# Optimization experiments

Measured on AMD Instinct MI355X. Metric: run time of the kernel, lower is better.

Reference implementation:

```python
import jax, jax.numpy as jnp
import numpy as np

B, N = 2048, 100            # batch, n_atoms
NC2 = N * (N - 1) // 2      # 4950 strictly-lower-triangle pairs

# Row-major strictly-lower-triangle indices: (1,0),(2,0),(2,1),(3,0),...
# This matches tf.where over band_part(index_matrix,-1,0)-diag in Triangle.
_TRIL_R, _TRIL_C = np.tril_indices(N, k=-1)


def setup_inputs() -> dict:
    key = jax.random.key(0)
    k1, k2 = jax.random.split(key)
    coords = jax.random.normal(k1, (B, N, 3), dtype=jnp.float32)
    decompFE_flat = jax.random.normal(k2, (B, NC2), dtype=jnp.float32)
    return {"coords": coords, "decompFE_flat": decompFE_flat}


def _triangle(flat):
    """[B, NC2] -> symmetric [B, N, N] with zero diagonal (Q + Q^T)."""
    b = flat.shape[0]
    m = jnp.zeros((b, N, N), dtype=flat.dtype).at[:, _TRIL_R, _TRIL_C].set(flat)
    return m + jnp.swapaxes(m, 1, 2)


def reference(coords, decompFE_flat):
    # Symmetric decomposed pairwise energies [B, N, N]
    decompFE = _triangle(decompFE_flat)

    # Pairwise squared distances [B, N, N]
    diff = coords[:, :, None, :] - coords[:, None, :, :]
    diff2 = jnp.sum(diff * diff, axis=-1)

    # Strictly-lower-triangle distances in row-major order [B, NC2]
    # (TF extracts nonzeros of the lower band; off-diagonal distances are
    #  nonzero for generic coords, so this is exactly the strict lower tri.)
    r_flat = jnp.sqrt(diff2[:, _TRIL_R, _TRIL_C])
    recip_r_flat = 1.0 / r_flat

    # Symmetric 1/r matrix, then einsum 'bijk,bij->bk' with k=1 == full ij sum
    Q3 = _triangle(recip_r_flat)
    E = jnp.sum(Q3 * decompFE, axis=(1, 2), keepdims=True)[:, :, 0] / 2.0  # [B,1]
    return E
```

## Files before the change

### kernel.cpp

```cpp
#include <hip/hip_runtime.h>


#define BATCH 2048
#define NATOMS 100
#define NPAIRS 4950
#define BLOCK 256

__global__ __launch_bounds__(BLOCK) void eij_kernel(
    const float* __restrict__ coords,
    const float* __restrict__ decomp,
    float* __restrict__ out)
{
    __shared__ float sx[NATOMS];
    __shared__ float sy[NATOMS];
    __shared__ float sz[NATOMS];
    __shared__ float wave_sums[BLOCK / 64];

    const int b = blockIdx.x;
    const int t = threadIdx.x;

    const float* cb = coords + (size_t)b * NATOMS * 3;
    for (int i = t; i < NATOMS; i += BLOCK) {
        sx[i] = cb[i * 3 + 0];
        sy[i] = cb[i * 3 + 1];
        sz[i] = cb[i * 3 + 2];
    }
    __syncthreads();

    const float* db = decomp + (size_t)b * NPAIRS;
    float acc = 0.0f;

    for (int p = t; p < NPAIRS; p += BLOCK) {
        int i = (int)((1.0f + sqrtf(8.0f * (float)p + 1.0f)) * 0.5f);
        while (i * (i - 1) / 2 > p) --i;
        while ((i + 1) * i / 2 <= p) ++i;
        const int j = p - i * (i - 1) / 2;

        const float dx = sx[i] - sx[j];
        const float dy = sy[i] - sy[j];
        const float dz = sz[i] - sz[j];
        const float d2 = dx * dx + dy * dy + dz * dz;
        acc += db[p] * rsqrtf(d2);
    }

    #pragma unroll
    for (int off = 32; off > 0; off >>= 1)
        acc += __shfl_down(acc, off, 64);

    const int wave = t >> 6;
    const int lane = t & 63;
    if (lane == 0) wave_sums[wave] = acc;
    __syncthreads();

    if (t == 0) {
        float s = 0.0f;
        #pragma unroll
        for (int w = 0; w < BLOCK / 64; ++w) s += wave_sums[w];
        out[b] = s;
    }
}

extern "C" void kernel_launch(void* const* d_in, const int* in_sizes, int n_in,
                              void* d_out, int out_size, void* d_ws, size_t ws_size,
                              hipStream_t stream) {
    const float* coords = (const float*)d_in[0];
    const float* decomp = (const float*)d_in[1];
    float* out = (float*)d_out;

    eij_kernel<<<BATCH, BLOCK, 0, stream>>>(coords, decomp, out);
}
```

Baseline: 91.34 us.

## Replace per-pair index solve with constexpr pair table and unroll loads

Precomputes a compile-time table mapping each flat pair index to packed (i,j) bytes, which replaces the sqrt plus correction-loop inversion done per element. Atom coordinates are stored as float4 in shared memory so each atom needs one LDS read. The pair loop is fully unrolled to a fixed 20 iterations with predicated tail handling so loads can be issued early. The cost is extra global/constant reads of the 16-bit table and higher register pressure from unrolling.

```diff
diff --git a/kernel.cpp b/kernel.cpp
--- a/kernel.cpp
+++ b/kernel.cpp
@@ -5,59 +5,69 @@
 #define NATOMS 100
 #define NPAIRS 4950
 #define BLOCK 256
+#define KMAX 20
+
+struct PairTab { unsigned short v[NPAIRS]; };
+
+__host__ __device__ constexpr PairTab make_tab() {
+    PairTab t{};
+    int p = 0;
+    for (int i = 1; i < NATOMS; ++i)
+        for (int j = 0; j < i; ++j)
+            t.v[p++] = (unsigned short)((i << 8) | j);
+    return t;
+}
+
+__device__ constexpr PairTab PAIR_TAB = make_tab();
 
 __global__ __launch_bounds__(BLOCK) void eij_kernel(
     const float* __restrict__ coords,
     const float* __restrict__ decomp,
     float* __restrict__ out)
 {
-    __shared__ float sx[NATOMS];
-    __shared__ float sy[NATOMS];
-    __shared__ float sz[NATOMS];
+    __shared__ float4 satom[NATOMS];
     __shared__ float wave_sums[BLOCK / 64];
 
     const int b = blockIdx.x;
     const int t = threadIdx.x;
 
     const float* cb = coords + (size_t)b * NATOMS * 3;
-    for (int i = t; i < NATOMS; i += BLOCK) {
-        sx[i] = cb[i * 3 + 0];
-        sy[i] = cb[i * 3 + 1];
-        sz[i] = cb[i * 3 + 2];
+    if (t < NATOMS) {
+        satom[t] = make_float4(cb[t * 3 + 0], cb[t * 3 + 1], cb[t * 3 + 2], 0.0f);
     }
     __syncthreads();
 
     const float* db = decomp + (size_t)b * NPAIRS;
     float acc = 0.0f;
 
-    for (int p = t; p < NPAIRS; p += BLOCK) {
-        int i = (int)((1.0f + sqrtf(8.0f * (float)p + 1.0f)) * 0.5f);
-        while (i * (i - 1) / 2 > p) --i;
-        while ((i + 1) * i / 2 <= p) ++i;
-        const int j = p - i * (i - 1) / 2;
-
-        const float dx = sx[i] - sx[j];
-        const float dy = sy[i] - sy[j];
-        const float dz = sz[i] - sz[j];
+    #pragma unroll
+    for (int k = 0; k < KMAX; ++k) {
+        const int p = t + (k << 8);
+        const bool ok = (p < NPAIRS);
+        const int pp = ok ? p : 0;
+        const float d = db[pp];
+        const unsigned pr = PAIR_TAB.v[pp];
+        const int i = (int)(pr >> 8);
+        const int j = (int)(pr & 255u);
+        const float4 ci = satom[i];
+        const float4 cj = satom[j];
+        const float dx = ci.x - cj.x;
+        const float dy = ci.y - cj.y;
+        const float dz = ci.z - cj.z;
         const float d2 = dx * dx + dy * dy + dz * dz;
-        acc += db[p] * rsqrtf(d2);
+        const float contrib = d * rsqrtf(d2);
+        acc += ok ? contrib : 0.0f;
     }
 
     #pragma unroll
     for (int off = 32; off > 0; off >>= 1)
         acc += __shfl_down(acc, off, 64);
 
-    const int wave = t >> 6;
-    const int lane = t & 63;
-    if (lane == 0) wave_sums[wave] = acc;
+    if ((t & 63) == 0) wave_sums[t >> 6] = acc;
     __syncthreads();
 
-    if (t == 0) {
-        float s = 0.0f;
-        #pragma unroll
-        for (int w = 0; w < BLOCK / 64; ++w) s += wave_sums[w];
-        out[b] = s;
-    }
+    if (t == 0)
+        out[b] = wave_sums[0] + wave_sums[1] + wave_sums[2] + wave_sums[3];
 }
 
 extern "C" void kernel_launch(void* const* d_in, const int* in_sizes, int n_in,
```

Measured after the change: 81.98 us. -10.2%, faster.

## Map waves to triangle rows and lanes to columns, dropping index inversion

Applied to the files above, without the earlier changes.

The per-pair sqrt-based triangular index inversion is replaced by a row-per-wave loop: each wave takes rows i strided by the wave count, and each lane handles columns lane and lane+64. Each lane keeps its two j-atom coordinates in registers, and row coordinates come from a shared-memory broadcast. This removes the sqrt, the correction loops and the scattered LDS gathers for j. In exchange, short rows leave lanes idle, and the work across waves is somewhat unbalanced.

```diff
diff --git a/kernel.cpp b/kernel.cpp
--- a/kernel.cpp
+++ b/kernel.cpp
@@ -5,59 +5,62 @@
 #define NATOMS 100
 #define NPAIRS 4950
 #define BLOCK 256
+#define NWAVES (BLOCK / 64)
 
 __global__ __launch_bounds__(BLOCK) void eij_kernel(
     const float* __restrict__ coords,
     const float* __restrict__ decomp,
     float* __restrict__ out)
 {
-    __shared__ float sx[NATOMS];
-    __shared__ float sy[NATOMS];
-    __shared__ float sz[NATOMS];
-    __shared__ float wave_sums[BLOCK / 64];
+    __shared__ float sx[NATOMS], sy[NATOMS], sz[NATOMS];
+    __shared__ float wave_sums[NWAVES];
 
     const int b = blockIdx.x;
     const int t = threadIdx.x;
+    const int wave = t >> 6;
+    const int lane = t & 63;
 
     const float* cb = coords + (size_t)b * NATOMS * 3;
-    for (int i = t; i < NATOMS; i += BLOCK) {
-        sx[i] = cb[i * 3 + 0];
-        sy[i] = cb[i * 3 + 1];
-        sz[i] = cb[i * 3 + 2];
+    for (int a = t; a < NATOMS; a += BLOCK) {
+        sx[a] = cb[a * 3 + 0];
+        sy[a] = cb[a * 3 + 1];
+        sz[a] = cb[a * 3 + 2];
     }
     __syncthreads();
+
+    const int j1 = (lane + 64 < NATOMS) ? (lane + 64) : (NATOMS - 1);
+    const float x0 = sx[lane], y0 = sy[lane], z0 = sz[lane];
+    const float x1 = sx[j1],   y1 = sy[j1],   z1 = sz[j1];
 
     const float* db = decomp + (size_t)b * NPAIRS;
     float acc = 0.0f;
 
-    for (int p = t; p < NPAIRS; p += BLOCK) {
-        int i = (int)((1.0f + sqrtf(8.0f * (float)p + 1.0f)) * 0.5f);
-        while (i * (i - 1) / 2 > p) --i;
-        while ((i + 1) * i / 2 <= p) ++i;
-        const int j = p - i * (i - 1) / 2;
+    for (int i = wave + 1; i < NATOMS; i += NWAVES) {
+        const int base = i * (i - 1) / 2;
+        const float cix = sx[i];
+        const float ciy = sy[i];
+        const float ciz = sz[i];
 
-        const float dx = sx[i] - sx[j];
-        const float dy = sy[i] - sy[j];
-        const float dz = sz[i] - sz[j];
-        const float d2 = dx * dx + dy * dy + dz * dz;
-        acc += db[p] * rsqrtf(d2);
+        if (lane < i) {
+            const float d = db[base + lane];
+            const float dx = cix - x0, dy = ciy - y0, dz = ciz - z0;
+            acc += d * rsqrtf(dx * dx + dy * dy + dz * dz);
+        }
+        if (lane + 64 < i) {
+            const float d = db[base + 64 + lane];
+            const float dx = cix - x1, dy = ciy - y1, dz = ciz - z1;
+            acc += d * rsqrtf(dx * dx + dy * dy + dz * dz);
+        }
     }
 
     #pragma unroll
     for (int off = 32; off > 0; off >>= 1)
         acc += __shfl_down(acc, off, 64);
-
-    const int wave = t >> 6;
-    const int lane = t & 63;
     if (lane == 0) wave_sums[wave] = acc;
     __syncthreads();
 
-    if (t == 0) {
-        float s = 0.0f;
-        #pragma unroll
-        for (int w = 0; w < BLOCK / 64; ++w) s += wave_sums[w];
-        out[b] = s;
-    }
+    if (t == 0)
+        out[b] = wave_sums[0] + wave_sums[1] + wave_sums[2] + wave_sums[3];
 }
 
 extern "C" void kernel_launch(void* const* d_in, const int* in_sizes, int n_in,
```

Result: faster. 87.67 us (-4.0%).
